# Performance work log

Measured on AMD Instinct MI355X. Metric: run time of the kernel, lower is better.

The kernel has to match this reference:

```python
import jax, jax.numpy as jnp
import numpy as np

B, S, LATENT = 256, 64, 20
U_DIM = LATENT // 5            # 4
T_HID, T_DEPTH = 20, 4         # treatment MLP
D_HID, D_DEPTH = 4 * LATENT, 4 # drift MLP (80 hidden)
T_LEN = 41
DT = 0.05
SIGMA, THETA, MU = 0.5, 1.0, 0.0
N = B * S
DIM_AUG = LATENT + 2           # latent + logqp + Tx


def _mlp(x, w_in, b_in, w_h, b_h, w_out, b_out, act):
    # input layer always ReLU (MLPSimple), hidden layers use `act`
    h = jax.nn.relu(x @ w_in.T + b_in)
    for i in range(w_h.shape[0]):
        h = act(h @ w_h[i].T + b_h[i])
    return h @ w_out.T + b_out


def setup_inputs() -> dict:
    key = jax.random.key(0)
    ks = jax.random.split(key, 20)

    def lin(k, out_d, in_d):
        bound = 1.0 / np.sqrt(in_d)
        return jax.random.uniform(k, (out_d, in_d), jnp.float32, -bound, bound)

    def bias(k, out_d, in_d):
        bound = 1.0 / np.sqrt(in_d)
        return jax.random.uniform(k, (out_d,), jnp.float32, -bound, bound)

    return {
        "z_SDE": jax.random.normal(ks[0], (B, S, LATENT), jnp.float32),
        "t": jnp.arange(T_LEN, dtype=jnp.float32) * DT,
        "Tx": jax.random.uniform(ks[1], (B,), jnp.float32),
        "noise": jax.random.normal(ks[2], (T_LEN - 1, N, DIM_AUG), jnp.float32),
        # treatment MLP: 1 -> 20 (ReLU) -> [20->20 ReLU]x4 -> 4
        "tw_in": lin(ks[3], T_HID, 1),
        "tb_in": bias(ks[4], T_HID, 1),
        "tw_h": jnp.stack([lin(jax.random.fold_in(ks[5], i), T_HID, T_HID) for i in range(T_DEPTH)]),
        "tb_h": jnp.stack([bias(jax.random.fold_in(ks[6], i), T_HID, T_HID) for i in range(T_DEPTH)]),
        "tw_out": lin(ks[7], U_DIM, T_HID),
        "tb_out": bias(ks[8], U_DIM, T_HID),
        # drift MLP: 24 -> 80 (ReLU) -> [80->80 Tanh]x4 -> 20
        "dw_in": lin(ks[9], D_HID, LATENT + U_DIM),
        "db_in": bias(ks[10], D_HID, LATENT + U_DIM),
        "dw_h": jnp.stack([lin(jax.random.fold_in(ks[11], i), D_HID, D_HID) for i in range(D_DEPTH)]),
        "db_h": jnp.stack([bias(jax.random.fold_in(ks[12], i), D_HID, D_HID) for i in range(D_DEPTH)]),
        "dw_out": lin(ks[13], LATENT, D_HID),
        "db_out": bias(ks[14], LATENT, D_HID),
    }


def reference(z_SDE, t, Tx, noise, tw_in, tb_in, tw_h, tb_h, tw_out, tb_out,
              dw_in, db_in, dw_h, db_h, dw_out, db_out):
    # build augmented initial state: [z, logqp0=0, Tx]  -> [N, DIM_AUG]
    Tx_rep = jnp.broadcast_to(Tx[:, None, None], (B, S, 1))
    aug_y0 = jnp.concatenate(
        [z_SDE, jnp.zeros((B, S, 1), z_SDE.dtype), Tx_rep.astype(z_SDE.dtype)], axis=-1
    ).reshape(N, DIM_AUG)

    dt = t[1] - t[0]           # 0.05, aligned with euler dt
    sqrt_dt = jnp.sqrt(dt)
    # diagonal diffusion: sigma on latent dims, 0 on (logqp, Tx) aug dims
    g_diag = jnp.concatenate([jnp.full((LATENT,), SIGMA, jnp.float32), jnp.zeros((2,), jnp.float32)])

    def f_aug(ti, y_aug):
        T_ = y_aug[:, -1]                     # treatment indicator
        y = y_aug[:, :LATENT]
        t_col = jnp.broadcast_to(ti, (N, 1)).astype(y.dtype)
        u = _mlp(t_col, tw_in, tb_in, tw_h, tb_h, tw_out, tb_out, jax.nn.relu)
        u_t = u * T_[:, None]
        h = THETA * (MU - y)                  # prior drift
        f = _mlp(jnp.concatenate([y, u_t], axis=-1), dw_in, db_in, dw_h, db_h, dw_out, db_out, jnp.tanh) - h
        # _stable_division(f - h, g); g = sigma = 0.5 > eps so plain division
        uu = (f - h) / SIGMA
        f_logqp = 0.5 * jnp.sum(uu * uu, axis=1, keepdims=True)
        return jnp.concatenate([f, f_logqp, jnp.zeros_like(f_logqp)], axis=1)

    def step(y, inp):
        ti, dW = inp
        y_new = y + f_aug(ti, y) * dt + g_diag[None, :] * (dW * sqrt_dt)
        return y_new, y_new

    _, ys_rest = jax.lax.scan(step, aug_y0, (t[:-1], noise))
    aug_ys = jnp.concatenate([aug_y0[None], ys_rest], axis=0)   # [T, N, DIM_AUG]
    # faithful to source: raw reshape of [T, N, dim] into [B, S, T, dim]
    aug_ys = aug_ys.reshape(-1, S, T_LEN, DIM_AUG)
    ys = aug_ys[:, :, :, :-2]
    logqp = aug_ys[:, :, -1, -2]
    return ys, logqp
```

## Files before the change

### kernel.cpp

```cpp
#include <hip/hip_runtime.h>
#include <math.h>
#include <stdint.h>

#define NPART 16384
#define NSTEP 40
#define DIMA  22
#define OUT0_ELEMS 13434880
#define TRAJ_OFF   160

typedef __attribute__((ext_vector_type(8))) short short8;
typedef __attribute__((ext_vector_type(4))) float floatx4;
typedef __attribute__((ext_vector_type(4))) int   intx4;
typedef __attribute__((ext_vector_type(2))) int   intx2;

union V4 { intx4 i; short8 s; floatx4 f; };

#define AIN_B   0
#define AH_B    5120
#define AOUT_B  56320
#define U_B     61440
#define LDS_BYTES 62080
#define STAGE_DW  15360

__device__ __forceinline__ uint32_t pk2(float a0, float a1) {
    uint32_t r;
    asm("v_cvt_pk_bf16_f32 %0, %1, %2" : "=v"(r) : "v"(a0), "v"(a1));
    return r;
}
__device__ __forceinline__ float fast_tanh(float x) {
    float e = __expf(2.0f * x);
    return 1.0f - 2.0f * __builtin_amdgcn_rcpf(e + 1.0f);
}

__global__ __launch_bounds__(256, 1) void sde_mfma(
    const float* __restrict__ z,      const float* __restrict__ t_arr,
    const float* __restrict__ Tx,     const float* __restrict__ noise,
    const float* __restrict__ dw_in,  const float* __restrict__ db_in,
    const float* __restrict__ dw_h,   const float* __restrict__ db_h,
    const float* __restrict__ dw_out, const float* __restrict__ db_out,
    const float* __restrict__ tw_in,  const float* __restrict__ tb_in,
    const float* __restrict__ tw_h,   const float* __restrict__ tb_h,
    const float* __restrict__ tw_out, const float* __restrict__ tb_out,
    float* __restrict__ out0,         float* __restrict__ traj)
{
    __shared__ __align__(16) uint8_t lds[LDS_BYTES];
    const int tid = threadIdx.x;

    for (int di = tid; di < STAGE_DW; di += 256) {
        uint32_t val = 0u;
        if (di < 1280) {
            int r = di & 255, lane = r >> 2, w = r & 3;
            int m = lane & 15, q = lane >> 4, mt = di >> 8;
            int f = -1;
            if (w < 2)            f = 4 * q + 2 * w;
            else if (q == 0)      f = 16 + 2 * (w - 2);
            else if (q == 1)      f = 20 + 2 * (w - 2);
            if (f >= 0) val = pk2(dw_in[(mt * 16 + m) * 24 + f],
                                  dw_in[(mt * 16 + m) * 24 + f + 1]);
        } else if (di < 14080) {
            int q2 = di - 1280, g = q2 / 640, r = q2 % 640;
            int l = g / 5, mt = g % 5;
            int lane, f;
            if (r < 512) {
                int kt = r >> 8, rr = r & 255, w = rr & 3;
                lane = rr >> 2;
                f = 16 * (2 * kt + (w >> 1)) + 4 * (lane >> 4) + 2 * (w & 1);
            } else {
                int rr = r - 512, d = rr & 1;
                lane = rr >> 1;
                f = 64 + 4 * (lane >> 4) + 2 * d;
            }
            int m = lane & 15;
            val = pk2(dw_h[l * 6400 + (mt * 16 + m) * 80 + f],
                      dw_h[l * 6400 + (mt * 16 + m) * 80 + f + 1]);
        } else {
            int q2 = di - 14080, mt = q2 / 640, r = q2 % 640;
            int lane, f;
            if (r < 512) {
                int kt = r >> 8, rr = r & 255, w = rr & 3;
                lane = rr >> 2;
                f = 16 * (2 * kt + (w >> 1)) + 4 * (lane >> 4) + 2 * (w & 1);
            } else {
                int rr = r - 512, d = rr & 1;
                lane = rr >> 1;
                f = 64 + 4 * (lane >> 4) + 2 * d;
            }
            int m = mt * 16 + (lane & 15);
            if (m < 20) val = pk2(dw_out[m * 80 + f], dw_out[m * 80 + f + 1]);
        }
        ((uint32_t*)lds)[di] = val;
    }
    if (tid < NSTEP) {
        float ti = t_arr[tid];
        float hh[20], h2[20];
        #pragma unroll
        for (int j = 0; j < 20; j++) {
            float v = tw_in[j] * ti + tb_in[j];
            hh[j] = v > 0.f ? v : 0.f;
        }
        #pragma unroll
        for (int l = 0; l < 4; l++) {
            #pragma unroll
            for (int j = 0; j < 20; j++) {
                float a = tb_h[l * 20 + j];
                #pragma unroll
                for (int k = 0; k < 20; k++) a += tw_h[(l * 20 + j) * 20 + k] * hh[k];
                h2[j] = a > 0.f ? a : 0.f;
            }
            #pragma unroll
            for (int j = 0; j < 20; j++) hh[j] = h2[j];
        }
        #pragma unroll
        for (int c = 0; c < 4; c++) {
            float a = tb_out[c];
            #pragma unroll
            for (int k = 0; k < 20; k++) a += tw_out[c * 20 + k] * hh[k];
            ((float*)(lds + U_B))[tid * 4 + c] = a;
        }
    }

    const int lane = tid & 63;
    const int n15  = lane & 15;
    const int quad = lane >> 4;
    const int wv   = tid >> 6;
    const int n    = blockIdx.x * 64 + wv * 16 + n15;
    const float Txb = Tx[blockIdx.x];
    const float dtv = t_arr[1] - t_arr[0];
    const float sdt = sqrtf(dtv);

    floatx4 cIn[5], cH[4][5], cOut[2];
    #pragma unroll
    for (int mt = 0; mt < 5; mt++)
        cIn[mt] = *(const floatx4*)(db_in + mt * 16 + quad * 4);
    #pragma unroll
    for (int l = 0; l < 4; l++)
        #pragma unroll
        for (int mt = 0; mt < 5; mt++)
            cH[l][mt] = *(const floatx4*)(db_h + l * 80 + mt * 16 + quad * 4);
    cOut[0] = *(const floatx4*)(db_out + quad * 4);
    cOut[1] = (quad == 0) ? *(const floatx4*)(db_out + 16)
                          : (floatx4){0.f, 0.f, 0.f, 0.f};
    __syncthreads();

    float y0[4], y1[4] = {0.f, 0.f, 0.f, 0.f};
    {
        floatx4 zv = *(const floatx4*)(z + (size_t)n * 20 + quad * 4);
        #pragma unroll
        for (int r = 0; r < 4; r++) y0[r] = zv[r];
        *(floatx4*)(out0 + (size_t)n * 20 + quad * 4) = zv;
        if (quad == 0) {
            floatx4 z2 = *(const floatx4*)(z + (size_t)n * 20 + 16);
            #pragma unroll
            for (int r = 0; r < 4; r++) y1[r] = z2[r];
            *(floatx4*)(out0 + (size_t)n * 20 + 16) = z2;
            traj[n] = 0.f;
        }
    }

    double lq = 0.0;
    for (int i = 0; i < NSTEP; i++) {
        size_t nbase = ((size_t)i * NPART + n) * DIMA;
        floatx4 dW0 = *(const floatx4*)(noise + nbase + quad * 4);
        floatx4 dW1 = {0.f, 0.f, 0.f, 0.f};
        if (quad == 0) dW1 = *(const floatx4*)(noise + nbase + 16);

        const floatx4 uv = *(const floatx4*)((const float*)(lds + U_B) + i * 4);
        float ut0 = uv[0] * Txb, ut1 = uv[1] * Txb;
        float ut2 = uv[2] * Txb, ut3 = uv[3] * Txb;

        V4 bin;
        bin.i[0] = pk2(y0[0], y0[1]);
        bin.i[1] = pk2(y0[2], y0[3]);
        if (quad == 0)      { bin.i[2] = pk2(y1[0], y1[1]); bin.i[3] = pk2(y1[2], y1[3]); }
        else if (quad == 1) { bin.i[2] = pk2(ut0, ut1);     bin.i[3] = pk2(ut2, ut3); }
        else                { bin.i[2] = 0;                 bin.i[3] = 0; }

        floatx4 acc[5];
        #pragma unroll
        for (int mt = 0; mt < 5; mt++) {
            V4 a; a.i = *(const intx4*)(lds + AIN_B + mt * 1024 + lane * 16);
            acc[mt] = __builtin_amdgcn_mfma_f32_16x16x32_bf16(a.s, bin.s, cIn[mt], 0, 0, 0);
        }
        uint32_t pkA[5][2];
        #pragma unroll
        for (int mt = 0; mt < 5; mt++) {
            pkA[mt][0] = pk2(fmaxf(acc[mt][0], 0.f), fmaxf(acc[mt][1], 0.f));
            pkA[mt][1] = pk2(fmaxf(acc[mt][2], 0.f), fmaxf(acc[mt][3], 0.f));
        }

        #pragma unroll
        for (int l = 0; l < 4; l++) {
            V4 b0, b1, b2;
            b0.i = (intx4){(int)pkA[0][0], (int)pkA[0][1], (int)pkA[1][0], (int)pkA[1][1]};
            b1.i = (intx4){(int)pkA[2][0], (int)pkA[2][1], (int)pkA[3][0], (int)pkA[3][1]};
            b2.i = (intx4){(int)pkA[4][0], (int)pkA[4][1], 0, 0};
            #pragma unroll
            for (int mt = 0; mt < 5; mt++) {
                const uint8_t* grp = lds + AH_B + (size_t)(l * 5 + mt) * 2560;
                V4 a0; a0.i = *(const intx4*)(grp + lane * 16);
                V4 a1; a1.i = *(const intx4*)(grp + 1024 + lane * 16);
                intx2 h2 = *(const intx2*)(grp + 2048 + lane * 8);
                V4 a2; a2.i = (intx4){h2[0], h2[1], 0, 0};
                floatx4 c = cH[l][mt];
                c = __builtin_amdgcn_mfma_f32_16x16x32_bf16(a0.s, b0.s, c, 0, 0, 0);
                c = __builtin_amdgcn_mfma_f32_16x16x32_bf16(a1.s, b1.s, c, 0, 0, 0);
                c = __builtin_amdgcn_mfma_f32_16x16x32_bf16(a2.s, b2.s, c, 0, 0, 0);
                acc[mt] = c;
            }
            #pragma unroll
            for (int mt = 0; mt < 5; mt++) {
                pkA[mt][0] = pk2(fast_tanh(acc[mt][0]), fast_tanh(acc[mt][1]));
                pkA[mt][1] = pk2(fast_tanh(acc[mt][2]), fast_tanh(acc[mt][3]));
            }
        }

        V4 b0, b1, b2;
        b0.i = (intx4){(int)pkA[0][0], (int)pkA[0][1], (int)pkA[1][0], (int)pkA[1][1]};
        b1.i = (intx4){(int)pkA[2][0], (int)pkA[2][1], (int)pkA[3][0], (int)pkA[3][1]};
        b2.i = (intx4){(int)pkA[4][0], (int)pkA[4][1], 0, 0};
        floatx4 oacc[2];
        #pragma unroll
        for (int mt = 0; mt < 2; mt++) {
            const uint8_t* grp = lds + AOUT_B + (size_t)mt * 2560;
            V4 a0; a0.i = *(const intx4*)(grp + lane * 16);
            V4 a1; a1.i = *(const intx4*)(grp + 1024 + lane * 16);
            intx2 h2 = *(const intx2*)(grp + 2048 + lane * 8);
            V4 a2; a2.i = (intx4){h2[0], h2[1], 0, 0};
            floatx4 c = cOut[mt];
            c = __builtin_amdgcn_mfma_f32_16x16x32_bf16(a0.s, b0.s, c, 0, 0, 0);
            c = __builtin_amdgcn_mfma_f32_16x16x32_bf16(a1.s, b1.s, c, 0, 0, 0);
            oacc[mt] = __builtin_amdgcn_mfma_f32_16x16x32_bf16(a2.s, b2.s, c, 0, 0, 0);
        }

        float part = 0.f;
        size_t obase = ((size_t)(i + 1) * NPART + n) * 20;
        floatx4 st;
        #pragma unroll
        for (int r = 0; r < 4; r++) {
            float o = oacc[0][r];
            float y = y0[r];
            float f = o + y;
            float uu = 2.f * o + 4.f * y;
            part += uu * uu;
            y0[r] = y + f * dtv + (0.5f * sdt) * dW0[r];
            st[r] = y0[r];
        }
        *(floatx4*)(out0 + obase + quad * 4) = st;
        if (quad == 0) {
            floatx4 st2;
            #pragma unroll
            for (int r = 0; r < 4; r++) {
                float o = oacc[1][r];
                float y = y1[r];
                float f = o + y;
                float uu = 2.f * o + 4.f * y;
                part += uu * uu;
                y1[r] = y + f * dtv + (0.5f * sdt) * dW1[r];
                st2[r] = y1[r];
            }
            *(floatx4*)(out0 + obase + 16) = st2;
        }
        part += __shfl_xor(part, 16);
        part += __shfl_xor(part, 32);
        lq += 0.5 * (double)part * (double)dtv;
        if (quad == 0) traj[(size_t)(i + 1) * NPART + n] = (float)lq;
    }
}

__global__ void gather_logqp(const float* __restrict__ traj, float* __restrict__ out1) {
    int i = blockIdx.x * 256 + threadIdx.x;
    if (i < NPART) out1[i] = traj[(size_t)41 * i + 40];
}

extern "C" void kernel_launch(void* const* d_in, const int* in_sizes, int n_in,
                              void* d_out, int out_size, void* d_ws, size_t ws_size,
                              hipStream_t stream) {
    const float* z      = (const float*)d_in[0];
    const float* t_arr  = (const float*)d_in[1];
    const float* Tx     = (const float*)d_in[2];
    const float* noise  = (const float*)d_in[3];
    const float* tw_in  = (const float*)d_in[4];
    const float* tb_in  = (const float*)d_in[5];
    const float* tw_h   = (const float*)d_in[6];
    const float* tb_h   = (const float*)d_in[7];
    const float* tw_out = (const float*)d_in[8];
    const float* tb_out = (const float*)d_in[9];
    const float* dw_in  = (const float*)d_in[10];
    const float* db_in  = (const float*)d_in[11];
    const float* dw_h   = (const float*)d_in[12];
    const float* db_h   = (const float*)d_in[13];
    const float* dw_out = (const float*)d_in[14];
    const float* db_out = (const float*)d_in[15];

    float* wsf  = (float*)d_ws;
    float* traj = wsf + TRAJ_OFF;
    float* out0 = (float*)d_out;
    float* out1 = out0 + OUT0_ELEMS;

    hipLaunchKernelGGL(sde_mfma, dim3(256), dim3(256), 0, stream,
                       z, t_arr, Tx, noise, dw_in, db_in, dw_h, db_h,
                       dw_out, db_out, tw_in, tb_in, tw_h, tb_h, tw_out, tb_out,
                       out0, traj);
    hipLaunchKernelGGL(gather_logqp, dim3(64), dim3(256), 0, stream, traj, out1);
}
```

Measured before the change: 259.4 us.

## Fold biases into MFMA padding and keep weight fragments resident in registers

Biases of the input, hidden and output layers are packed into the unused K-padding slot of the weight fragments, and a constant 1.0 is placed in the matching activation slot. Accumulators then start from zero instead of preloaded bias vectors. All weight fragments are loaded from LDS once before the time loop and kept in registers, removing per-step LDS reads. This greatly raises register pressure, which risks spills or lower occupancy, and biases are now rounded to bf16.

```diff
diff --git a/kernel.cpp b/kernel.cpp
--- a/kernel.cpp
+++ b/kernel.cpp
@@ -55,8 +55,9 @@
             if (w < 2)            f = 4 * q + 2 * w;
             else if (q == 0)      f = 16 + 2 * (w - 2);
             else if (q == 1)      f = 20 + 2 * (w - 2);
-            if (f >= 0) val = pk2(dw_in[(mt * 16 + m) * 24 + f],
-                                  dw_in[(mt * 16 + m) * 24 + f + 1]);
+            if (f >= 0)               val = pk2(dw_in[(mt * 16 + m) * 24 + f],
+                                                dw_in[(mt * 16 + m) * 24 + f + 1]);
+            else if (q == 2 && w == 2) val = pk2(db_in[mt * 16 + m], 0.f);
         } else if (di < 14080) {
             int q2 = di - 1280, g = q2 / 640, r = q2 % 640;
             int l = g / 5, mt = g % 5;
@@ -128,19 +129,41 @@
     const float dtv = t_arr[1] - t_arr[0];
     const float sdt = sqrtf(dtv);
 
-    floatx4 cIn[5], cH[4][5], cOut[2];
+    __syncthreads();
+
+    V4 aIn[5];
     #pragma unroll
     for (int mt = 0; mt < 5; mt++)
-        cIn[mt] = *(const floatx4*)(db_in + mt * 16 + quad * 4);
+        aIn[mt].i = *(const intx4*)(lds + AIN_B + mt * 1024 + lane * 16);
+
+    V4 aH0[20], aH1[20], aH2[20];
     #pragma unroll
-    for (int l = 0; l < 4; l++)
-        #pragma unroll
-        for (int mt = 0; mt < 5; mt++)
-            cH[l][mt] = *(const floatx4*)(db_h + l * 80 + mt * 16 + quad * 4);
-    cOut[0] = *(const floatx4*)(db_out + quad * 4);
-    cOut[1] = (quad == 0) ? *(const floatx4*)(db_out + 16)
-                          : (floatx4){0.f, 0.f, 0.f, 0.f};
-    __syncthreads();
+    for (int l = 0; l < 4; l++) {
+        #pragma unroll
+        for (int mt = 0; mt < 5; mt++) {
+            const int g = l * 5 + mt;
+            const uint8_t* grp = lds + AH_B + (size_t)g * 2560;
+            aH0[g].i = *(const intx4*)(grp + lane * 16);
+            aH1[g].i = *(const intx4*)(grp + 1024 + lane * 16);
+            intx2 h2 = *(const intx2*)(grp + 2048 + lane * 8);
+            uint32_t bd = (quad == 0) ? pk2(db_h[l * 80 + mt * 16 + n15], 0.f) : 0u;
+            aH2[g].i = (intx4){h2[0], h2[1], (int)bd, 0};
+        }
+    }
+
+    V4 aO0[2], aO1[2], aO2[2];
+    #pragma unroll
+    for (int mt = 0; mt < 2; mt++) {
+        const uint8_t* grp = lds + AOUT_B + (size_t)mt * 2560;
+        aO0[mt].i = *(const intx4*)(grp + lane * 16);
+        aO1[mt].i = *(const intx4*)(grp + 1024 + lane * 16);
+        intx2 h2 = *(const intx2*)(grp + 2048 + lane * 8);
+        int m = mt * 16 + n15;
+        uint32_t bd = (quad == 0 && m < 20) ? pk2(db_out[m], 0.f) : 0u;
+        aO2[mt].i = (intx4){h2[0], h2[1], (int)bd, 0};
+    }
+
+    const floatx4 zf = {0.f, 0.f, 0.f, 0.f};
 
     float y0[4], y1[4] = {0.f, 0.f, 0.f, 0.f};
     {
@@ -173,14 +196,13 @@
         bin.i[1] = pk2(y0[2], y0[3]);
         if (quad == 0)      { bin.i[2] = pk2(y1[0], y1[1]); bin.i[3] = pk2(y1[2], y1[3]); }
         else if (quad == 1) { bin.i[2] = pk2(ut0, ut1);     bin.i[3] = pk2(ut2, ut3); }
+        else if (quad == 2) { bin.i[2] = 0x00003F80;        bin.i[3] = 0; }
         else                { bin.i[2] = 0;                 bin.i[3] = 0; }
 
         floatx4 acc[5];
         #pragma unroll
-        for (int mt = 0; mt < 5; mt++) {
-            V4 a; a.i = *(const intx4*)(lds + AIN_B + mt * 1024 + lane * 16);
-            acc[mt] = __builtin_amdgcn_mfma_f32_16x16x32_bf16(a.s, bin.s, cIn[mt], 0, 0, 0);
-        }
+        for (int mt = 0; mt < 5; mt++)
+            acc[mt] = __builtin_amdgcn_mfma_f32_16x16x32_bf16(aIn[mt].s, bin.s, zf, 0, 0, 0);
         uint32_t pkA[5][2];
         #pragma unroll
         for (int mt = 0; mt < 5; mt++) {
@@ -193,18 +215,14 @@
             V4 b0, b1, b2;
             b0.i = (intx4){(int)pkA[0][0], (int)pkA[0][1], (int)pkA[1][0], (int)pkA[1][1]};
             b1.i = (intx4){(int)pkA[2][0], (int)pkA[2][1], (int)pkA[3][0], (int)pkA[3][1]};
-            b2.i = (intx4){(int)pkA[4][0], (int)pkA[4][1], 0, 0};
+            b2.i = (intx4){(int)pkA[4][0], (int)pkA[4][1], 0x00003F80, 0};
             #pragma unroll
             for (int mt = 0; mt < 5; mt++) {
-                const uint8_t* grp = lds + AH_B + (size_t)(l * 5 + mt) * 2560;
-                V4 a0; a0.i = *(const intx4*)(grp + lane * 16);
-                V4 a1; a1.i = *(const intx4*)(grp + 1024 + lane * 16);
-                intx2 h2 = *(const intx2*)(grp + 2048 + lane * 8);
-                V4 a2; a2.i = (intx4){h2[0], h2[1], 0, 0};
-                floatx4 c = cH[l][mt];
-                c = __builtin_amdgcn_mfma_f32_16x16x32_bf16(a0.s, b0.s, c, 0, 0, 0);
-                c = __builtin_amdgcn_mfma_f32_16x16x32_bf16(a1.s, b1.s, c, 0, 0, 0);
-                c = __builtin_amdgcn_mfma_f32_16x16x32_bf16(a2.s, b2.s, c, 0, 0, 0);
+                const int g = l * 5 + mt;
+                floatx4 c;
+                c = __builtin_amdgcn_mfma_f32_16x16x32_bf16(aH0[g].s, b0.s, zf, 0, 0, 0);
+                c = __builtin_amdgcn_mfma_f32_16x16x32_bf16(aH1[g].s, b1.s, c, 0, 0, 0);
+                c = __builtin_amdgcn_mfma_f32_16x16x32_bf16(aH2[g].s, b2.s, c, 0, 0, 0);
                 acc[mt] = c;
             }
             #pragma unroll
@@ -217,19 +235,14 @@
         V4 b0, b1, b2;
         b0.i = (intx4){(int)pkA[0][0], (int)pkA[0][1], (int)pkA[1][0], (int)pkA[1][1]};
         b1.i = (intx4){(int)pkA[2][0], (int)pkA[2][1], (int)pkA[3][0], (int)pkA[3][1]};
-        b2.i = (intx4){(int)pkA[4][0], (int)pkA[4][1], 0, 0};
+        b2.i = (intx4){(int)pkA[4][0], (int)pkA[4][1], 0x00003F80, 0};
         floatx4 oacc[2];
         #pragma unroll
         for (int mt = 0; mt < 2; mt++) {
-            const uint8_t* grp = lds + AOUT_B + (size_t)mt * 2560;
-            V4 a0; a0.i = *(const intx4*)(grp + lane * 16);
-            V4 a1; a1.i = *(const intx4*)(grp + 1024 + lane * 16);
-            intx2 h2 = *(const intx2*)(grp + 2048 + lane * 8);
-            V4 a2; a2.i = (intx4){h2[0], h2[1], 0, 0};
-            floatx4 c = cOut[mt];
-            c = __builtin_amdgcn_mfma_f32_16x16x32_bf16(a0.s, b0.s, c, 0, 0, 0);
-            c = __builtin_amdgcn_mfma_f32_16x16x32_bf16(a1.s, b1.s, c, 0, 0, 0);
-            oacc[mt] = __builtin_amdgcn_mfma_f32_16x16x32_bf16(a2.s, b2.s, c, 0, 0, 0);
+            floatx4 c;
+            c = __builtin_amdgcn_mfma_f32_16x16x32_bf16(aO0[mt].s, b0.s, zf, 0, 0, 0);
+            c = __builtin_amdgcn_mfma_f32_16x16x32_bf16(aO1[mt].s, b1.s, c, 0, 0, 0);
+            oacc[mt] = __builtin_amdgcn_mfma_f32_16x16x32_bf16(aO2[mt].s, b2.s, c, 0, 0, 0);
         }
 
         float part = 0.f;
```

New measurement: 259.7 us. Within noise of the previous version (+0.1%).
